# Kernel optimization log

Measured on AMD Instinct MI355X. Metric: run time of the kernel, lower is better.

The kernel has to match this reference:

```python
import jax, jax.numpy as jnp
import numpy as np

SPARSITY_RATIO = 0.3


def setup_inputs() -> dict:
    key = jax.random.key(0)
    adj = jax.random.normal(key, (8, 4096, 4096), dtype=jnp.float32)
    return {"adj": adj}


def reference(adj) -> jnp.ndarray:
    # training-mode path: keep top-k entries per row, zero the rest.
    n = adj.shape[-1]
    k = max(1, int(n * (1.0 - SPARSITY_RATIO)))
    # Per-row k-th largest value acts as the selection threshold.
    # With continuous random inputs ties have measure zero, so
    # (adj >= kth_val) selects exactly the same entries as
    # topk + scatter in the original torch code, without
    # materializing an index tensor or doing a scatter.
    topk_vals = jax.lax.top_k(adj, k)[0]        # [B, N, k]
    kth_val = topk_vals[..., -1:]               # [B, N, 1]
    return jnp.where(adj >= kth_val, adj, jnp.zeros((), dtype=adj.dtype))
```

## Files before the change

kernel.cpp:

```cpp
#include <hip/hip_runtime.h>


#define NCOL 4096
#define KSEL 2867

__global__ __launch_bounds__(256) void sparsify_kernel(const float* __restrict__ adj,
                                                       float* __restrict__ out) {
    __shared__ unsigned hist[4][256];
    __shared__ unsigned s_state[2];

    const int t    = threadIdx.x;
    const int wave = t >> 6;
    const int lane = t & 63;
    const size_t row = blockIdx.x;

    const float4* __restrict__ in4  = (const float4*)(adj + row * (size_t)NCOL);
    float4* __restrict__       out4 = (float4*)(out + row * (size_t)NCOL);

    float4 v[4];
    unsigned u[16];
#pragma unroll
    for (int i = 0; i < 4; ++i) v[i] = in4[t + 256 * i];
#pragma unroll
    for (int i = 0; i < 4; ++i) {
        unsigned bx = __float_as_uint(v[i].x);
        unsigned by = __float_as_uint(v[i].y);
        unsigned bz = __float_as_uint(v[i].z);
        unsigned bw = __float_as_uint(v[i].w);
        u[4*i+0] = bx ^ ((unsigned)((int)bx >> 31) | 0x80000000u);
        u[4*i+1] = by ^ ((unsigned)((int)by >> 31) | 0x80000000u);
        u[4*i+2] = bz ^ ((unsigned)((int)bz >> 31) | 0x80000000u);
        u[4*i+3] = bw ^ ((unsigned)((int)bw >> 31) | 0x80000000u);
    }

    if (t == 0) { s_state[0] = 0u; s_state[1] = KSEL; }

#pragma unroll
    for (int p = 0; p < 4; ++p) {
        const int shift = 24 - 8 * p;
        const unsigned mask = (p == 0) ? 0u : (0xFFFFFFFFu << (32 - 8 * p));

        ((uint4*)hist)[t] = make_uint4(0u, 0u, 0u, 0u);
        __syncthreads();

        const unsigned pref = s_state[0];
        const unsigned kr   = s_state[1];

#pragma unroll
        for (int i = 0; i < 16; ++i) {
            if ((u[i] & mask) == pref)
                atomicAdd(&hist[wave][(u[i] >> shift) & 0xFFu], 1u);
        }
        __syncthreads();

        if (wave == 0) {
            const uint4 a0 = *(const uint4*)&hist[0][4 * lane];
            const uint4 a1 = *(const uint4*)&hist[1][4 * lane];
            const uint4 a2 = *(const uint4*)&hist[2][4 * lane];
            const uint4 a3 = *(const uint4*)&hist[3][4 * lane];
            unsigned cc[4];
            cc[0] = a0.x + a1.x + a2.x + a3.x;
            cc[1] = a0.y + a1.y + a2.y + a3.y;
            cc[2] = a0.z + a1.z + a2.z + a3.z;
            cc[3] = a0.w + a1.w + a2.w + a3.w;
            unsigned s = cc[0] + cc[1] + cc[2] + cc[3];

            unsigned pscan = s;
#pragma unroll
            for (int d = 1; d < 64; d <<= 1) {
                unsigned nv = __shfl_up(pscan, d, 64);
                if (lane >= d) pscan += nv;
            }
            const unsigned total = __shfl(pscan, 63, 64);
            unsigned cum = total - pscan;

#pragma unroll
            for (int s2 = 3; s2 >= 0; --s2) {
                const unsigned nxt = cum + cc[s2];
                if (cum < kr && kr <= nxt) {
                    s_state[0] = pref | ((unsigned)(4 * lane + s2) << shift);
                    s_state[1] = kr - cum;
                }
                cum = nxt;
            }
        }
        __syncthreads();
    }

    const unsigned tu = s_state[0];
    const unsigned tb = (tu & 0x80000000u) ? (tu ^ 0x80000000u) : ~tu;
    const float thr = __uint_as_float(tb);

#pragma unroll
    for (int i = 0; i < 4; ++i) {
        float4 o;
        o.x = (v[i].x >= thr) ? v[i].x : 0.0f;
        o.y = (v[i].y >= thr) ? v[i].y : 0.0f;
        o.z = (v[i].z >= thr) ? v[i].z : 0.0f;
        o.w = (v[i].w >= thr) ? v[i].w : 0.0f;
        out4[t + 256 * i] = o;
    }
}

extern "C" void kernel_launch(void* const* d_in, const int* in_sizes, int n_in,
                              void* d_out, int out_size, void* d_ws, size_t ws_size,
                              hipStream_t stream) {
    const float* adj = (const float*)d_in[0];
    float* out = (float*)d_out;
    const int rows = in_sizes[0] / NCOL;
    sparsify_kernel<<<rows, 256, 0, stream>>>(adj, out);
}
```

Before: 865.5 us.

## Replace LDS radix-select with wave-per-row bitwise ballot binary search

Each row is now handled by a single wavefront rather than a whole 256-thread block, with four rows per block. The kernel finds the k-th largest value with a 32-step bitwise binary search on the order-preserving integer keys, counting matches with ballot and popcount. This removes the shared-memory histograms, the LDS atomics and the block-wide barriers of the 8-bit radix passes. The trade-offs are 32 full passes over the 64 keys each lane holds, higher register pressure (64 keys per lane), and recovering the float values from the keys instead of keeping the original loads.

```diff
diff --git a/kernel.cpp b/kernel.cpp
--- a/kernel.cpp
+++ b/kernel.cpp
@@ -4,101 +4,60 @@
 #define NCOL 4096
 #define KSEL 2867
 
-__global__ __launch_bounds__(256) void sparsify_kernel(const float* __restrict__ adj,
-                                                       float* __restrict__ out) {
-    __shared__ unsigned hist[4][256];
-    __shared__ unsigned s_state[2];
+__global__ __launch_bounds__(256, 4) void sparsify_kernel(const float* __restrict__ adj,
+                                                          float* __restrict__ out,
+                                                          int nrows) {
+    const int lane = threadIdx.x & 63;
+    const int wave = threadIdx.x >> 6;
+    const int row  = blockIdx.x * 4 + wave;
+    if (row >= nrows) return;
 
-    const int t    = threadIdx.x;
-    const int wave = t >> 6;
-    const int lane = t & 63;
-    const size_t row = blockIdx.x;
+    const float4* __restrict__ in4  = (const float4*)(adj + (size_t)row * NCOL);
+    float4* __restrict__       out4 = (float4*)(out + (size_t)row * NCOL);
 
-    const float4* __restrict__ in4  = (const float4*)(adj + row * (size_t)NCOL);
-    float4* __restrict__       out4 = (float4*)(out + row * (size_t)NCOL);
-
-    float4 v[4];
-    unsigned u[16];
+    unsigned u[64];
 #pragma unroll
-    for (int i = 0; i < 4; ++i) v[i] = in4[t + 256 * i];
-#pragma unroll
-    for (int i = 0; i < 4; ++i) {
-        unsigned bx = __float_as_uint(v[i].x);
-        unsigned by = __float_as_uint(v[i].y);
-        unsigned bz = __float_as_uint(v[i].z);
-        unsigned bw = __float_as_uint(v[i].w);
-        u[4*i+0] = bx ^ ((unsigned)((int)bx >> 31) | 0x80000000u);
-        u[4*i+1] = by ^ ((unsigned)((int)by >> 31) | 0x80000000u);
-        u[4*i+2] = bz ^ ((unsigned)((int)bz >> 31) | 0x80000000u);
-        u[4*i+3] = bw ^ ((unsigned)((int)bw >> 31) | 0x80000000u);
+    for (int c = 0; c < 16; ++c) {
+        const float4 v = in4[lane + 64 * c];
+        const unsigned bx = __float_as_uint(v.x);
+        const unsigned by = __float_as_uint(v.y);
+        const unsigned bz = __float_as_uint(v.z);
+        const unsigned bw = __float_as_uint(v.w);
+        u[4 * c + 0] = bx ^ ((unsigned)((int)bx >> 31) | 0x80000000u);
+        u[4 * c + 1] = by ^ ((unsigned)((int)by >> 31) | 0x80000000u);
+        u[4 * c + 2] = bz ^ ((unsigned)((int)bz >> 31) | 0x80000000u);
+        u[4 * c + 3] = bw ^ ((unsigned)((int)bw >> 31) | 0x80000000u);
     }
 
-    if (t == 0) { s_state[0] = 0u; s_state[1] = KSEL; }
-
+    unsigned cand = 0u;
+#pragma unroll 1
+    for (int b = 31; b >= 0; --b) {
+        const unsigned c2 = cand | (1u << b);
+        unsigned cnt = 0u;
 #pragma unroll
-    for (int p = 0; p < 4; ++p) {
-        const int shift = 24 - 8 * p;
-        const unsigned mask = (p == 0) ? 0u : (0xFFFFFFFFu << (32 - 8 * p));
-
-        ((uint4*)hist)[t] = make_uint4(0u, 0u, 0u, 0u);
-        __syncthreads();
-
-        const unsigned pref = s_state[0];
-        const unsigned kr   = s_state[1];
-
-#pragma unroll
-        for (int i = 0; i < 16; ++i) {
-            if ((u[i] & mask) == pref)
-                atomicAdd(&hist[wave][(u[i] >> shift) & 0xFFu], 1u);
-        }
-        __syncthreads();
-
-        if (wave == 0) {
-            const uint4 a0 = *(const uint4*)&hist[0][4 * lane];
-            const uint4 a1 = *(const uint4*)&hist[1][4 * lane];
-            const uint4 a2 = *(const uint4*)&hist[2][4 * lane];
-            const uint4 a3 = *(const uint4*)&hist[3][4 * lane];
-            unsigned cc[4];
-            cc[0] = a0.x + a1.x + a2.x + a3.x;
-            cc[1] = a0.y + a1.y + a2.y + a3.y;
-            cc[2] = a0.z + a1.z + a2.z + a3.z;
-            cc[3] = a0.w + a1.w + a2.w + a3.w;
-            unsigned s = cc[0] + cc[1] + cc[2] + cc[3];
-
-            unsigned pscan = s;
-#pragma unroll
-            for (int d = 1; d < 64; d <<= 1) {
-                unsigned nv = __shfl_up(pscan, d, 64);
-                if (lane >= d) pscan += nv;
-            }
-            const unsigned total = __shfl(pscan, 63, 64);
-            unsigned cum = total - pscan;
-
-#pragma unroll
-            for (int s2 = 3; s2 >= 0; --s2) {
-                const unsigned nxt = cum + cc[s2];
-                if (cum < kr && kr <= nxt) {
-                    s_state[0] = pref | ((unsigned)(4 * lane + s2) << shift);
-                    s_state[1] = kr - cum;
-                }
-                cum = nxt;
-            }
-        }
-        __syncthreads();
+        for (int i = 0; i < 64; ++i)
+            cnt += (unsigned)__popcll(__ballot(u[i] >= c2));
+        if (cnt >= KSEL) cand = c2;
     }
 
-    const unsigned tu = s_state[0];
-    const unsigned tb = (tu & 0x80000000u) ? (tu ^ 0x80000000u) : ~tu;
+    const unsigned tb = (cand & 0x80000000u) ? (cand ^ 0x80000000u) : ~cand;
     const float thr = __uint_as_float(tb);
 
 #pragma unroll
-    for (int i = 0; i < 4; ++i) {
+    for (int c = 0; c < 16; ++c) {
+        float f[4];
+#pragma unroll
+        for (int j = 0; j < 4; ++j) {
+            const unsigned uu = u[4 * c + j];
+            const unsigned bb = (uu & 0x80000000u) ? (uu ^ 0x80000000u) : ~uu;
+            f[j] = __uint_as_float(bb);
+        }
         float4 o;
-        o.x = (v[i].x >= thr) ? v[i].x : 0.0f;
-        o.y = (v[i].y >= thr) ? v[i].y : 0.0f;
-        o.z = (v[i].z >= thr) ? v[i].z : 0.0f;
-        o.w = (v[i].w >= thr) ? v[i].w : 0.0f;
-        out4[t + 256 * i] = o;
+        o.x = (f[0] >= thr) ? f[0] : 0.0f;
+        o.y = (f[1] >= thr) ? f[1] : 0.0f;
+        o.z = (f[2] >= thr) ? f[2] : 0.0f;
+        o.w = (f[3] >= thr) ? f[3] : 0.0f;
+        out4[lane + 64 * c] = o;
     }
 }
 
@@ -108,5 +67,6 @@
     const float* adj = (const float*)d_in[0];
     float* out = (float*)d_out;
     const int rows = in_sizes[0] / NCOL;
-    sparsify_kernel<<<rows, 256, 0, stream>>>(adj, out);
+    const int blocks = (rows + 3) / 4;
+    sparsify_kernel<<<blocks, 256, 0, stream>>>(adj, out, rows);
 }
```

Measured after the change: 988.2 us. 14.2% more time.
